# Kernel tuning notes

Hardware: AMD Instinct MI355X
Metric: run time of the kernel (lower is better)

## Reference

```python
import jax, jax.numpy as jnp
import numpy as np
import math

N = 100000      # n_entities
C = 128         # channel
E = 600000      # n_edges
NNZ = 1000000   # interact_mat nnz
NU = 50000      # n_users
NREL = 25       # n_relations
H = 4           # n_heads
DK = C // H     # d_k


def setup_inputs() -> dict:
    key = jax.random.key(0)
    ks = jax.random.split(key, 13)
    s = 1.0 / math.sqrt(C)
    return {
        "entity_emb": jax.random.normal(ks[0], (N, C), jnp.float32),
        "W_Q": jax.random.normal(ks[1], (C, C), jnp.float32) * s,
        "W_K": jax.random.normal(ks[2], (C, C), jnp.float32) * s,
        "W_V": jax.random.normal(ks[3], (C, C), jnp.float32) * s,
        "W_O": jax.random.normal(ks[4], (C, C), jnp.float32) * s,
        "relation_att": jax.random.normal(ks[5], (NREL - 1, H, DK, DK), jnp.float32) * s,
        "relation_msg": jax.random.normal(ks[6], (NREL - 1, H, DK, DK), jnp.float32) * s,
        "relation_emb": jax.random.normal(ks[7], (NREL - 1, C), jnp.float32),
        "edge_index": jax.random.randint(ks[8], (2, E), 0, N, jnp.int32),
        "edge_type": jax.random.randint(ks[9], (E,), 1, NREL, jnp.int32),
        "im_rows": jax.random.randint(ks[10], (NNZ,), 0, NU, jnp.int32),
        "im_cols": jax.random.randint(ks[11], (NNZ,), 0, N, jnp.int32),
        "im_vals": jax.random.uniform(ks[12], (NNZ,), jnp.float32),
        "n_users": NU,
    }


def reference(entity_emb, W_Q, W_K, W_V, W_O, relation_att, relation_msg,
              relation_emb, edge_index, edge_type, im_rows, im_cols, im_vals,
              n_users):
    n_entities, channel = entity_emb.shape
    n_heads, d_k = H, channel // H
    head, tail = edge_index[0], edge_index[1]
    rel = edge_type - 1

    # Step 1: heterogeneous mutual attention
    q = (entity_emb[head] @ W_Q).reshape(-1, n_heads, d_k)            # [E,H,Dk]
    k = (entity_emb[tail] @ W_K).reshape(-1, n_heads, d_k)
    k = jnp.einsum("ehd,ehdk->ehk", k, relation_att[rel])
    score = (q * k).sum(-1) / math.sqrt(d_k)                           # [E,H]

    # Step 2: heterogeneous message passing
    v = (entity_emb[tail] @ W_V).reshape(-1, n_heads, d_k)
    v = jnp.einsum("ehd,ehdk->ehk", v, relation_msg[rel])

    # scatter_softmax over target node id (head)
    seg_max = jax.ops.segment_max(score, head, num_segments=n_entities)  # [N,H]
    ex = jnp.exp(score - seg_max[head])
    denom = jax.ops.segment_sum(ex, head, num_segments=n_entities)
    attn = ex / denom[head]                                              # [E,H]

    agg = (v * attn[..., None]).reshape(-1, n_heads * d_k) @ W_O         # [E,C]
    entity_agg = jax.ops.segment_sum(agg, head, num_segments=n_entities)

    # user aggregate: sparse [NU,N] @ entity_emb
    user_agg = jax.ops.segment_sum(entity_emb[im_cols] * im_vals[:, None],
                                   im_rows, num_segments=n_users)
    return entity_agg, user_agg
```

## Files before the change

### kernel.cpp

```cpp
#include <hip/hip_runtime.h>
#include <hip/hip_bf16.h>
#include <math.h>

typedef __attribute__((ext_vector_type(8))) unsigned short u16x8;
typedef __attribute__((ext_vector_type(4))) unsigned short u16x4;
typedef __attribute__((ext_vector_type(8))) short bf16x8;
typedef __attribute__((ext_vector_type(4))) float f32x4;

#define NRELMAX 32

__device__ __forceinline__ float b2f(unsigned short u) {
    return __uint_as_float(((unsigned)u) << 16);
}
__device__ __forceinline__ unsigned short f2b(float v) {
    __hip_bfloat16 b = __float2bfloat16(v);
    return *reinterpret_cast<unsigned short*>(&b);
}

__device__ __forceinline__ bf16x8 lda_frag(const __hip_bfloat16* p) {
    return *(const bf16x8*)p;
}
__device__ __forceinline__ void st_o(__hip_bfloat16* p, float v) { *p = __float2bfloat16(v); }
__device__ __forceinline__ void st_o(float* p, float v) { *p = v; }

template <typename TO>
__global__ __launch_bounds__(256) void mfma_gemm(const __hip_bfloat16* __restrict__ A,
                                                 const __hip_bfloat16* __restrict__ Wt,
                                                 TO* __restrict__ out, int n)
{
    const int tid = threadIdx.x;
    const int w = tid >> 6;
    const int l = tid & 63;
    const int q = l >> 4;
    const int c16 = l & 15;
    const int wr = (w >> 1) * 64;
    const int wc = (w & 1) * 64;
    const long row0 = (long)blockIdx.x * 128;

    f32x4 acc[4][4] = {};
    #pragma unroll
    for (int ks = 0; ks < 4; ++ks) {
        bf16x8 af[4];
        #pragma unroll
        for (int rb = 0; rb < 4; ++rb) {
            long r = row0 + wr + rb * 16 + c16;
            if (r >= n) r = n - 1;
            af[rb] = lda_frag(A + r * 128 + ks * 32 + q * 8);
        }
        #pragma unroll
        for (int cb = 0; cb < 4; ++cb) {
            bf16x8 wf = *(const bf16x8*)(Wt + (size_t)(wc + cb * 16 + c16) * 128 + ks * 32 + q * 8);
            #pragma unroll
            for (int rb = 0; rb < 4; ++rb)
                acc[rb][cb] = __builtin_amdgcn_mfma_f32_16x16x32_bf16(af[rb], wf, acc[rb][cb], 0, 0, 0);
        }
    }
    #pragma unroll
    for (int rb = 0; rb < 4; ++rb) {
        #pragma unroll
        for (int r = 0; r < 4; ++r) {
            long row = row0 + wr + rb * 16 + q * 4 + r;
            if (row < n) {
                #pragma unroll
                for (int cb = 0; cb < 4; ++cb)
                    st_o(out + row * 128 + wc + cb * 16 + c16, acc[rb][cb][r]);
            }
        }
    }
}

__global__ __launch_bounds__(256) void trans_w4(
    const float* __restrict__ W0, const float* __restrict__ W1,
    const float* __restrict__ W2, const float* __restrict__ W3,
    __hip_bfloat16* __restrict__ T0, __hip_bfloat16* __restrict__ T1,
    __hip_bfloat16* __restrict__ T2, __hip_bfloat16* __restrict__ T3)
{
    int t = blockIdx.x * 256 + threadIdx.x;
    int w = t >> 14, r = t & 16383;
    const float* W = (w == 0) ? W0 : (w == 1) ? W1 : (w == 2) ? W2 : W3;
    __hip_bfloat16* T = (w == 0) ? T0 : (w == 1) ? T1 : (w == 2) ? T2 : T3;
    int k = r >> 7, c = r & 127;
    T[(size_t)c * 128 + k] = __float2bfloat16(W[(size_t)k * 128 + c]);
}

__global__ __launch_bounds__(256) void conv_emb(const float* __restrict__ emb,
                                                __hip_bfloat16* __restrict__ embb, long n4)
{
    long i = ((long)blockIdx.x * 256 + threadIdx.x) * 4;
    if (i >= n4 * 4) return;
    float4 v = *(const float4*)(emb + i);
    u16x4 o;
    o[0] = f2b(v.x); o[1] = f2b(v.y); o[2] = f2b(v.z); o[3] = f2b(v.w);
    *(u16x4*)(embb + i) = o;
}

__global__ __launch_bounds__(256) void conv_tab(const float* __restrict__ att,
                                                const float* __restrict__ msg,
                                                __hip_bfloat16* __restrict__ Atab,
                                                __hip_bfloat16* __restrict__ Mtab, int nrel)
{
    int t = blockIdx.x * 256 + threadIdx.x;
    int tot = nrel * 4096;
    if (t >= 2 * tot) return;
    const float* src = (t < tot) ? att : msg;
    __hip_bfloat16* dst = (t < tot) ? Atab : Mtab;
    int u = (t < tot) ? t : t - tot;
    int rel = u >> 12, rem = u & 4095;
    int h = rem >> 10;  rem &= 1023;
    int s2 = rem >> 9;  rem &= 511;
    int lane = rem >> 3, j = rem & 7;
    int g = lane >> 4, c = lane & 15;
    dst[u] = __float2bfloat16(src[(size_t)rel * 4096 + h * 1024 + s2 * 16 + (g * 8 + j) * 32 + c]);
}

__global__ __launch_bounds__(256) void count_rec(
    const int* __restrict__ head, const int* __restrict__ etyp,
    const int* __restrict__ irow,
    unsigned* __restrict__ ecnt8, unsigned* __restrict__ ucnt8,
    unsigned* __restrict__ rcnt, int* __restrict__ plocalE,
    int* __restrict__ plocalU, int E, int NNZ, int Np, int NUp)
{
    __shared__ unsigned lcnt[NRELMAX];
    const int tid = threadIdx.x;
    if (tid < NRELMAX) lcnt[tid] = 0;
    __syncthreads();
    int i = blockIdx.x * 256 + tid;
    unsigned rep = (unsigned)(blockIdx.x & 7);
    if (i < E) {
        unsigned p = atomicAdd(&ecnt8[rep * Np + head[i]], 1u);
        plocalE[i] = (int)(p | (rep << 28));
        atomicAdd(&lcnt[etyp[i] - 1], 1u);
    }
    if (i < NNZ) {
        unsigned p = atomicAdd(&ucnt8[rep * NUp + irow[i]], 1u);
        plocalU[i] = (int)(p | (rep << 28));
    }
    __syncthreads();
    if (tid < NRELMAX) {
        unsigned c = lcnt[tid];
        if (c) atomicAdd(&rcnt[tid], c);
    }
}

__global__ __launch_bounds__(256) void sum_rep(const unsigned* __restrict__ cnt8,
                                               unsigned* __restrict__ tot, int n, int stride)
{
    int i = blockIdx.x * 256 + threadIdx.x;
    if (i >= n) return;
    unsigned t = 0;
    #pragma unroll
    for (int r = 0; r < 8; ++r) t += cnt8[(size_t)r * stride + i];
    tot[i] = t;
}

__global__ __launch_bounds__(256) void mk_repbase(unsigned* __restrict__ cnt8,
                                                  const unsigned* __restrict__ base,
                                                  int n, int stride)
{
    int i = blockIdx.x * 256 + threadIdx.x;
    if (i >= n) return;
    unsigned acc = base[i];
    #pragma unroll
    for (int r = 0; r < 8; ++r) {
        unsigned c = cnt8[(size_t)r * stride + i];
        cnt8[(size_t)r * stride + i] = acc;
        acc += c;
    }
}

__global__ void rel_scan(const unsigned* __restrict__ rcnt, unsigned* __restrict__ rcur,
                         unsigned* __restrict__ rend, unsigned* __restrict__ rnext, int nrel)
{
    if (threadIdx.x == 0 && blockIdx.x == 0) {
        unsigned acc = 0;
        for (int r = 0; r < nrel; ++r) {
            rcur[r] = acc;
            rend[r] = acc + rcnt[r];
            acc += (rcnt[r] + 15u) & ~15u;
            rnext[r] = acc;
        }
    }
}

__global__ __launch_bounds__(256) void fill_pads(const unsigned* __restrict__ rend,
                                                 const unsigned* __restrict__ rnext,
                                                 int4* __restrict__ emeta, int nrel, long emax)
{
    for (int r = 0; r < nrel; ++r) {
        unsigned s = rend[r], e2 = rnext[r];
        for (unsigned i = s + threadIdx.x; i < e2; i += 256)
            emeta[i] = make_int4(0, 0, -1, r);
    }
    long ep = rnext[nrel - 1];
    for (long i = ep + threadIdx.x; i < emax; i += 256)
        emeta[i] = make_int4(0, 0, -1, nrel - 1);
}

__global__ __launch_bounds__(1024) void scan1(const unsigned* __restrict__ in,
                                              unsigned* __restrict__ out,
                                              unsigned* __restrict__ bsum, int n)
{
    __shared__ unsigned sh[1024];
    int i = blockIdx.x * 1024 + threadIdx.x;
    unsigned v = (i < n) ? in[i] : 0u;
    sh[threadIdx.x] = v;
    __syncthreads();
    for (int off = 1; off < 1024; off <<= 1) {
        unsigned t = (threadIdx.x >= (unsigned)off) ? sh[threadIdx.x - off] : 0u;
        __syncthreads();
        sh[threadIdx.x] += t;
        __syncthreads();
    }
    if (i < n) out[i] = sh[threadIdx.x] - v;
    if (threadIdx.x == 1023) bsum[blockIdx.x] = sh[1023];
}

__global__ __launch_bounds__(1024) void scan2(unsigned* __restrict__ bsum, int nb)
{
    __shared__ unsigned sh[1024];
    unsigned v = (threadIdx.x < (unsigned)nb) ? bsum[threadIdx.x] : 0u;
    sh[threadIdx.x] = v;
    __syncthreads();
    for (int off = 1; off < 1024; off <<= 1) {
        unsigned t = (threadIdx.x >= (unsigned)off) ? sh[threadIdx.x - off] : 0u;
        __syncthreads();
        sh[threadIdx.x] += t;
        __syncthreads();
    }
    if (threadIdx.x < (unsigned)nb) bsum[threadIdx.x] = sh[threadIdx.x] - v;
}

__global__ __launch_bounds__(1024) void scan3(unsigned* __restrict__ out,
                                              const unsigned* __restrict__ bsum, int n)
{
    int i = blockIdx.x * 1024 + threadIdx.x;
    if (i < n) out[i] += bsum[blockIdx.x];
}

__global__ __launch_bounds__(256) void fill_user2(const int* __restrict__ irow,
                                                  const int* __restrict__ icol,
                                                  const float* __restrict__ ival,
                                                  const unsigned* __restrict__ repbaseU,
                                                  const int* __restrict__ plocalU,
                                                  int2* __restrict__ upair, int n, int NUp)
{
    int i = blockIdx.x * 256 + threadIdx.x;
    if (i >= n) return;
    unsigned pl = (unsigned)plocalU[i];
    unsigned rep = pl >> 28;
    unsigned pos = pl & 0x0FFFFFFFu;
    unsigned slot = repbaseU[(size_t)rep * NUp + irow[i]] + pos;
    upair[slot] = make_int2(icol[i], __float_as_int(ival[i]));
}

__global__ __launch_bounds__(256) void fill_both2(const int* __restrict__ head,
                                                  const int* __restrict__ tail,
                                                  const int* __restrict__ etyp,
                                                  const unsigned* __restrict__ repbaseE,
                                                  const int* __restrict__ plocalE,
                                                  unsigned* __restrict__ rcur,
                                                  int4* __restrict__ emeta, int n, int Np)
{
    __shared__ unsigned lcnt[NRELMAX];
    __shared__ unsigned lbase[NRELMAX];
    const int tid = threadIdx.x;
    if (tid < NRELMAX) lcnt[tid] = 0;
    __syncthreads();
    int i = blockIdx.x * 256 + tid;
    int r = 0;
    unsigned lpos = 0;
    if (i < n) {
        r = etyp[i] - 1;
        lpos = atomicAdd(&lcnt[r], 1u);
    }
    __syncthreads();
    if (tid < NRELMAX) {
        unsigned c = lcnt[tid];
        lbase[tid] = c ? atomicAdd(&rcur[tid], c) : 0u;
    }
    __syncthreads();
    if (i < n) {
        unsigned pl = (unsigned)plocalE[i];
        unsigned rep = pl >> 28;
        unsigned pos = pl & 0x0FFFFFFFu;
        int hn = head[i];
        unsigned slot = repbaseE[(size_t)rep * Np + hn] + pos;
        emeta[lbase[r] + lpos] = make_int4(hn, tail[i], (int)slot, r);
    }
}

template <int ROUND>
__global__ __launch_bounds__(256, 2) void edge_pass(
    const __hip_bfloat16* __restrict__ Qb, const __hip_bfloat16* __restrict__ Kb,
    const __hip_bfloat16* __restrict__ Vb,
    const __hip_bfloat16* __restrict__ Atab, const __hip_bfloat16* __restrict__ Mtab,
    const int4* __restrict__ emeta, float* __restrict__ SC,
    __hip_bfloat16* __restrict__ VPh, long Epad, int chunk)
{
    const int wv = (blockIdx.x * 256 + threadIdx.x) >> 6;
    const int l = threadIdx.x & 63;
    const int g = l >> 4;
    const int c = l & 15;
    long j0 = (long)wv * chunk;
    if (j0 >= Epad) return;
    long j1 = j0 + chunk; if (j1 > Epad) j1 = Epad;

    bf16x8 aK[2][2], aM[2][2];
    int currel = -1;
    for (long pos = j0; pos < j1; pos += 16) {
        const int4 md = emeta[pos + c];
        const int rel0 = __shfl(md.w, 0, 64);
        if (rel0 != currel) {
            currel = rel0;
            #pragma unroll
            for (int hl = 0; hl < 2; ++hl) {
                const int h = ROUND * 2 + hl;
                #pragma unroll
                for (int s2 = 0; s2 < 2; ++s2) {
                    size_t idx = ((((size_t)rel0 * 4 + h) * 2 + s2) * 64 + l) * 8;
                    aK[hl][s2] = *(const bf16x8*)(Atab + idx);
                    aM[hl][s2] = *(const bf16x8*)(Mtab + idx);
                }
            }
        }
        const int tn = md.y, hn = md.x, slot = md.z;
        #pragma unroll
        for (int hl = 0; hl < 2; ++hl) {
            const int h = ROUND * 2 + hl;
            bf16x8 bk = *(const bf16x8*)(Kb + (size_t)tn * 128 + h * 32 + g * 8);
            bf16x8 bv = *(const bf16x8*)(Vb + (size_t)tn * 128 + h * 32 + g * 8);
            f32x4 z = {0.f, 0.f, 0.f, 0.f};
            f32x4 klo = __builtin_amdgcn_mfma_f32_16x16x32_bf16(aK[hl][0], bk, z, 0, 0, 0);
            f32x4 khi = __builtin_amdgcn_mfma_f32_16x16x32_bf16(aK[hl][1], bk, z, 0, 0, 0);
            f32x4 vlo = __builtin_amdgcn_mfma_f32_16x16x32_bf16(aM[hl][0], bv, z, 0, 0, 0);
            f32x4 vhi = __builtin_amdgcn_mfma_f32_16x16x32_bf16(aM[hl][1], bv, z, 0, 0, 0);
            const __hip_bfloat16* qp = Qb + (size_t)hn * 128 + h * 32;
            u16x4 q1 = *(const u16x4*)(qp + g * 4);
            u16x4 q2 = *(const u16x4*)(qp + 16 + g * 4);
            float p = 0.f;
            #pragma unroll
            for (int r = 0; r < 4; ++r)
                p += b2f(q1[r]) * klo[r] + b2f(q2[r]) * khi[r];
            p += __shfl_xor(p, 16, 64);
            p += __shfl_xor(p, 32, 64);
            if (slot >= 0) {
                if (g == 0) SC[(size_t)slot * 4 + h] = p * 0.17677669529663687f;
                u16x4 plo, phi;
                #pragma unroll
                for (int r = 0; r < 4; ++r) { plo[r] = f2b(vlo[r]); phi[r] = f2b(vhi[r]); }
                __hip_bfloat16* dst = VPh + (size_t)slot * 64 + hl * 32;
                *(u16x4*)(dst + g * 4) = plo;
                *(u16x4*)(dst + 16 + g * 4) = phi;
            }
        }
    }
}

template <int ROUND>
__global__ __launch_bounds__(256) void node_pass(
    const float* __restrict__ SC, const __hip_bfloat16* __restrict__ VPh,
    const unsigned* __restrict__ estart, __hip_bfloat16* __restrict__ M, int n, int Etot)
{
    int node = (blockIdx.x * 256 + threadIdx.x) >> 6;
    if (node >= n) return;
    int l = threadIdx.x & 63;
    int half = l >> 5;
    const int h = ROUND * 2 + half;
    unsigned beg = estart[node];
    unsigned end = (node + 1 < n) ? estart[node + 1] : (unsigned)Etot;
    float mx = -INFINITY, dn = 0.f;
    for (unsigned j = beg; j < end; ++j) {
        float s = SC[(size_t)j * 4 + h];
        float m2 = fmaxf(mx, s);
        dn = dn * __expf(mx - m2) + __expf(s - m2);
        mx = m2;
    }
    float inv = (end > beg) ? 1.f / dn : 0.f;
    float acc = 0.f;
    for (unsigned j = beg; j < end; ++j) {
        float w = __expf(SC[(size_t)j * 4 + h] - mx) * inv;
        acc = fmaf(w, __bfloat162float(VPh[(size_t)j * 64 + l]), acc);
    }
    M[(size_t)node * 128 + ROUND * 64 + l] = __float2bfloat16(acc);
}

__global__ __launch_bounds__(256) void user_gather(
    const __hip_bfloat16* __restrict__ embb, const unsigned* __restrict__ ustart,
    const int2* __restrict__ upair, float* __restrict__ out, int nu, int NNZ)
{
    int u = (blockIdx.x * 256 + threadIdx.x) >> 5;
    if (u >= nu) return;
    int l = threadIdx.x & 31;
    unsigned beg = ustart[u];
    unsigned end = (u + 1 < nu) ? ustart[u + 1] : (unsigned)NNZ;
    float a0 = 0.f, a1 = 0.f, a2 = 0.f, a3 = 0.f;
    float b0 = 0.f, b1 = 0.f, b2 = 0.f, b3 = 0.f;
    unsigned j = beg;
    for (; j + 3 < end; j += 4) {
        int2 p0 = upair[j], p1 = upair[j + 1], p2 = upair[j + 2], p3 = upair[j + 3];
        float v0 = __int_as_float(p0.y), v1 = __int_as_float(p1.y);
        float v2 = __int_as_float(p2.y), v3 = __int_as_float(p3.y);
        uint2 e0 = *(const uint2*)((const unsigned*)(embb + (size_t)p0.x * 128) + l * 2);
        uint2 e1 = *(const uint2*)((const unsigned*)(embb + (size_t)p1.x * 128) + l * 2);
        uint2 e2 = *(const uint2*)((const unsigned*)(embb + (size_t)p2.x * 128) + l * 2);
        uint2 e3 = *(const uint2*)((const unsigned*)(embb + (size_t)p3.x * 128) + l * 2);
        a0 = fmaf(b2f((unsigned short)(e0.x & 0xFFFF)), v0, a0);
        a1 = fmaf(b2f((unsigned short)(e0.x >> 16)), v0, a1);
        a2 = fmaf(b2f((unsigned short)(e0.y & 0xFFFF)), v0, a2);
        a3 = fmaf(b2f((unsigned short)(e0.y >> 16)), v0, a3);
        b0 = fmaf(b2f((unsigned short)(e1.x & 0xFFFF)), v1, b0);
        b1 = fmaf(b2f((unsigned short)(e1.x >> 16)), v1, b1);
        b2 = fmaf(b2f((unsigned short)(e1.y & 0xFFFF)), v1, b2);
        b3 = fmaf(b2f((unsigned short)(e1.y >> 16)), v1, b3);
        a0 = fmaf(b2f((unsigned short)(e2.x & 0xFFFF)), v2, a0);
        a1 = fmaf(b2f((unsigned short)(e2.x >> 16)), v2, a1);
        a2 = fmaf(b2f((unsigned short)(e2.y & 0xFFFF)), v2, a2);
        a3 = fmaf(b2f((unsigned short)(e2.y >> 16)), v2, a3);
        b0 = fmaf(b2f((unsigned short)(e3.x & 0xFFFF)), v3, b0);
        b1 = fmaf(b2f((unsigned short)(e3.x >> 16)), v3, b1);
        b2 = fmaf(b2f((unsigned short)(e3.y & 0xFFFF)), v3, b2);
        b3 = fmaf(b2f((unsigned short)(e3.y >> 16)), v3, b3);
    }
    for (; j < end; ++j) {
        int2 p0 = upair[j];
        float v0 = __int_as_float(p0.y);
        uint2 e0 = *(const uint2*)((const unsigned*)(embb + (size_t)p0.x * 128) + l * 2);
        a0 = fmaf(b2f((unsigned short)(e0.x & 0xFFFF)), v0, a0);
        a1 = fmaf(b2f((unsigned short)(e0.x >> 16)), v0, a1);
        a2 = fmaf(b2f((unsigned short)(e0.y & 0xFFFF)), v0, a2);
        a3 = fmaf(b2f((unsigned short)(e0.y >> 16)), v0, a3);
    }
    *(float4*)(out + (size_t)u * 128 + l * 4) =
        make_float4(a0 + b0, a1 + b1, a2 + b2, a3 + b3);
}

extern "C" void kernel_launch(void* const* d_in, const int* in_sizes, int n_in,
                              void* d_out, int out_size, void* d_ws, size_t ws_size,
                              hipStream_t stream)
{
    const float* emb = (const float*)d_in[0];
    const float* W_Q = (const float*)d_in[1];
    const float* W_K = (const float*)d_in[2];
    const float* W_V = (const float*)d_in[3];
    const float* W_O = (const float*)d_in[4];
    const float* att = (const float*)d_in[5];
    const float* msg = (const float*)d_in[6];
    const int* eidx  = (const int*)d_in[8];
    const int* etyp  = (const int*)d_in[9];
    const int* irow  = (const int*)d_in[10];
    const int* icol  = (const int*)d_in[11];
    const float* ival = (const float*)d_in[12];

    const int N    = in_sizes[0] / 128;
    const int E    = in_sizes[8] / 2;
    const int NNZ  = in_sizes[10];
    const int NU   = out_size / 128 - N;
    const int NREL = in_sizes[5] / 4096;

    const int* head = eidx;
    const int* tail = eidx + E;

    const int Np  = (N + 255) & ~255;
    const int NUp = (NU + 255) & ~255;

    const size_t NC = (size_t)N * 128;
    char* p = (char*)d_ws;
    __hip_bfloat16* VPh = (__hip_bfloat16*)p; p += (size_t)E * 64 * 2;
    __hip_bfloat16* Kb  = (__hip_bfloat16*)p; p += NC * 2;
    __hip_bfloat16* Vb  = (__hip_bfloat16*)p; p += NC * 2;
    __hip_bfloat16* M   = (__hip_bfloat16*)p; p += NC * 2;
    unsigned* rcnt  = (unsigned*)p; p += 32 * 4;
    unsigned* rcur  = (unsigned*)p; p += 32 * 4;
    unsigned* rend  = (unsigned*)p; p += 32 * 4;
    unsigned* rnext = (unsigned*)p; p += 32 * 4;
    unsigned* ucnt  = (unsigned*)p; p += (size_t)NUp * 4;
    unsigned* bsum  = (unsigned*)p; p += 1024 * 4;
    unsigned* bsumU = (unsigned*)p; p += 1024 * 4;
    int2* upair     = (int2*)p;     p += (size_t)NNZ * 8;
    __hip_bfloat16* WtQ = (__hip_bfloat16*)p; p += 16384 * 2;
    __hip_bfloat16* WtK = (__hip_bfloat16*)p; p += 16384 * 2;
    __hip_bfloat16* WtV = (__hip_bfloat16*)p; p += 16384 * 2;
    __hip_bfloat16* WtO = (__hip_bfloat16*)p; p += 16384 * 2;
    __hip_bfloat16* Atab = (__hip_bfloat16*)p; p += (size_t)NREL * 4096 * 2;
    __hip_bfloat16* Mtab = (__hip_bfloat16*)p; p += (size_t)NREL * 4096 * 2;

    int* plocalU     = (int*)VPh;
    int* plocalE     = plocalU + NNZ;
    unsigned* ucnt8  = (unsigned*)(plocalE + E);
    unsigned* ecnt8  = ucnt8 + (size_t)8 * NUp;

    float* out_ent = (float*)d_out;
    float* out_usr = out_ent + NC;
    __hip_bfloat16* embb = (__hip_bfloat16*)out_ent;
    __hip_bfloat16* Qb   = (__hip_bfloat16*)((char*)d_out + NC * 2);
    const long Emax = E + 512;
    float* SC   = out_usr;
    int4* emeta = (int4*)(out_usr + (size_t)E * 4);
    unsigned* ecnt = (unsigned*)((char*)emeta + (size_t)Emax * 16);

    hipMemsetAsync(rcnt, 0, 32 * 4, stream);
    hipMemsetAsync(ucnt8, 0, ((size_t)8 * NUp + (size_t)8 * Np) * 4, stream);

    trans_w4<<<256, 256, 0, stream>>>(W_Q, W_K, W_V, W_O, WtQ, WtK, WtV, WtO);
    conv_emb<<<(int)((NC / 4 + 255) / 256), 256, 0, stream>>>(emb, embb, (long)(NC / 4));
    conv_tab<<<(2 * NREL * 4096 + 255) / 256, 256, 0, stream>>>(att, msg, Atab, Mtab, NREL);

    int gg = (N + 127) / 128;
    mfma_gemm<__hip_bfloat16><<<gg, 256, 0, stream>>>(embb, WtQ, Qb, N);
    mfma_gemm<__hip_bfloat16><<<gg, 256, 0, stream>>>(embb, WtK, Kb, N);
    mfma_gemm<__hip_bfloat16><<<gg, 256, 0, stream>>>(embb, WtV, Vb, N);

    int gmax = ((NNZ > E ? NNZ : E) + 255) / 256;
    count_rec<<<gmax, 256, 0, stream>>>(head, etyp, irow, ecnt8, ucnt8, rcnt,
                                        plocalE, plocalU, E, NNZ, Np, NUp);
    rel_scan<<<1, 64, 0, stream>>>(rcnt, rcur, rend, rnext, NREL);
    fill_pads<<<1, 256, 0, stream>>>(rend, rnext, emeta, NREL, Emax);

    sum_rep<<<(N + 255) / 256, 256, 0, stream>>>(ecnt8, ecnt, N, Np);
    sum_rep<<<(NU + 255) / 256, 256, 0, stream>>>(ucnt8, ucnt, NU, NUp);
    int nbE = (N + 1023) / 1024;
    scan1<<<nbE, 1024, 0, stream>>>(ecnt, ecnt, bsum, N);
    scan2<<<1, 1024, 0, stream>>>(bsum, nbE);
    scan3<<<nbE, 1024, 0, stream>>>(ecnt, bsum, N);
    int nbU = (NU + 1023) / 1024;
    scan1<<<nbU, 1024, 0, stream>>>(ucnt, ucnt, bsumU, NU);
    scan2<<<1, 1024, 0, stream>>>(bsumU, nbU);
    scan3<<<nbU, 1024, 0, stream>>>(ucnt, bsumU, NU);
    mk_repbase<<<(N + 255) / 256, 256, 0, stream>>>(ecnt8, ecnt, N, Np);
    mk_repbase<<<(NU + 255) / 256, 256, 0, stream>>>(ucnt8, ucnt, NU, NUp);

    fill_user2<<<(NNZ + 255) / 256, 256, 0, stream>>>(irow, icol, ival, ucnt8,
                                                      plocalU, upair, NNZ, NUp);
    fill_both2<<<(E + 255) / 256, 256, 0, stream>>>(head, tail, etyp, ecnt8,
                                                    plocalE, rcur, emeta, E, Np);

    const int NWAVE = 16384;
    int chunk = (int)(((Emax + NWAVE - 1) / NWAVE + 15) & ~15L);
    edge_pass<0><<<NWAVE / 4, 256, 0, stream>>>(Qb, Kb, Vb, Atab, Mtab, emeta, SC, VPh, Emax, chunk);
    node_pass<0><<<(N + 3) / 4, 256, 0, stream>>>(SC, VPh, ecnt, M, N, E);
    edge_pass<1><<<NWAVE / 4, 256, 0, stream>>>(Qb, Kb, Vb, Atab, Mtab, emeta, SC, VPh, Emax, chunk);
    node_pass<1><<<(N + 3) / 4, 256, 0, stream>>>(SC, VPh, ecnt, M, N, E);

    user_gather<<<(NU + 7) / 8, 256, 0, stream>>>(embb, ucnt, upair, out_usr, NU, NNZ);

    mfma_gemm<float><<<gg, 256, 0, stream>>>(M, WtO, out_ent, N);
}
```

Before: 637.0 us.

## Fuse preprocessing, QKV GEMMs, scans and fills into fewer launches

Fuses the weight transpose, relation-table conversion, embedding bf16 conversion and edge/user counting into one block-partitioned kernel. The three QKV GEMMs become a single launch, and the multi-kernel block scans plus the relation scan become one three-block scan kernel. The user and edge fills and the pad fill are merged into one kernel. It also drops the 8-way replicated counters in favour of direct atomics on the count arrays. The goal is to cut launch count and the extra replica-sum passes, at the cost of more atomic contention and a serial single-block scan per array.

```diff
diff --git a/kernel.cpp b/kernel.cpp
--- a/kernel.cpp
+++ b/kernel.cpp
@@ -1,6 +1,7 @@
 #include <hip/hip_runtime.h>
 #include <hip/hip_bf16.h>
 #include <math.h>
+
 
 typedef __attribute__((ext_vector_type(8))) unsigned short u16x8;
 typedef __attribute__((ext_vector_type(4))) unsigned short u16x4;
@@ -24,9 +25,9 @@
 __device__ __forceinline__ void st_o(float* p, float v) { *p = v; }
 
 template <typename TO>
-__global__ __launch_bounds__(256) void mfma_gemm(const __hip_bfloat16* __restrict__ A,
-                                                 const __hip_bfloat16* __restrict__ Wt,
-                                                 TO* __restrict__ out, int n)
+__device__ __forceinline__ void gemm_body(const __hip_bfloat16* __restrict__ A,
+                                          const __hip_bfloat16* __restrict__ Wt,
+                                          TO* __restrict__ out, int n, int blk)
 {
     const int tid = threadIdx.x;
     const int w = tid >> 6;
@@ -35,7 +36,7 @@
     const int c16 = l & 15;
     const int wr = (w >> 1) * 64;
     const int wc = (w & 1) * 64;
-    const long row0 = (long)blockIdx.x * 128;
+    const long row0 = (long)blk * 128;
 
     f32x4 acc[4][4] = {};
     #pragma unroll
@@ -69,71 +70,91 @@
     }
 }
 
-__global__ __launch_bounds__(256) void trans_w4(
+template <typename TO>
+__global__ __launch_bounds__(256) void mfma_gemm(const __hip_bfloat16* __restrict__ A,
+                                                 const __hip_bfloat16* __restrict__ Wt,
+                                                 TO* __restrict__ out, int n)
+{
+    gemm_body<TO>(A, Wt, out, n, blockIdx.x);
+}
+
+__global__ __launch_bounds__(256) void qkv3(const __hip_bfloat16* __restrict__ A,
+                                            const __hip_bfloat16* __restrict__ WtQ,
+                                            const __hip_bfloat16* __restrict__ WtK,
+                                            const __hip_bfloat16* __restrict__ WtV,
+                                            __hip_bfloat16* __restrict__ Qb,
+                                            __hip_bfloat16* __restrict__ Kb,
+                                            __hip_bfloat16* __restrict__ Vb, int n, int gg)
+{
+    int which = blockIdx.x / gg;
+    int blk = blockIdx.x % gg;
+    const __hip_bfloat16* Wt = (which == 0) ? WtQ : (which == 1) ? WtK : WtV;
+    __hip_bfloat16* Out = (which == 0) ? Qb : (which == 1) ? Kb : Vb;
+    gemm_body<__hip_bfloat16>(A, Wt, Out, n, blk);
+}
+
+__global__ __launch_bounds__(256) void prep_count(
     const float* __restrict__ W0, const float* __restrict__ W1,
     const float* __restrict__ W2, const float* __restrict__ W3,
     __hip_bfloat16* __restrict__ T0, __hip_bfloat16* __restrict__ T1,
-    __hip_bfloat16* __restrict__ T2, __hip_bfloat16* __restrict__ T3)
-{
-    int t = blockIdx.x * 256 + threadIdx.x;
-    int w = t >> 14, r = t & 16383;
-    const float* W = (w == 0) ? W0 : (w == 1) ? W1 : (w == 2) ? W2 : W3;
-    __hip_bfloat16* T = (w == 0) ? T0 : (w == 1) ? T1 : (w == 2) ? T2 : T3;
-    int k = r >> 7, c = r & 127;
-    T[(size_t)c * 128 + k] = __float2bfloat16(W[(size_t)k * 128 + c]);
-}
-
-__global__ __launch_bounds__(256) void conv_emb(const float* __restrict__ emb,
-                                                __hip_bfloat16* __restrict__ embb, long n4)
-{
-    long i = ((long)blockIdx.x * 256 + threadIdx.x) * 4;
-    if (i >= n4 * 4) return;
-    float4 v = *(const float4*)(emb + i);
-    u16x4 o;
-    o[0] = f2b(v.x); o[1] = f2b(v.y); o[2] = f2b(v.z); o[3] = f2b(v.w);
-    *(u16x4*)(embb + i) = o;
-}
-
-__global__ __launch_bounds__(256) void conv_tab(const float* __restrict__ att,
-                                                const float* __restrict__ msg,
-                                                __hip_bfloat16* __restrict__ Atab,
-                                                __hip_bfloat16* __restrict__ Mtab, int nrel)
-{
-    int t = blockIdx.x * 256 + threadIdx.x;
-    int tot = nrel * 4096;
-    if (t >= 2 * tot) return;
-    const float* src = (t < tot) ? att : msg;
-    __hip_bfloat16* dst = (t < tot) ? Atab : Mtab;
-    int u = (t < tot) ? t : t - tot;
-    int rel = u >> 12, rem = u & 4095;
-    int h = rem >> 10;  rem &= 1023;
-    int s2 = rem >> 9;  rem &= 511;
-    int lane = rem >> 3, j = rem & 7;
-    int g = lane >> 4, c = lane & 15;
-    dst[u] = __float2bfloat16(src[(size_t)rel * 4096 + h * 1024 + s2 * 16 + (g * 8 + j) * 32 + c]);
-}
-
-__global__ __launch_bounds__(256) void count_rec(
+    __hip_bfloat16* __restrict__ T2, __hip_bfloat16* __restrict__ T3,
+    const float* __restrict__ att, const float* __restrict__ msg,
+    __hip_bfloat16* __restrict__ Atab, __hip_bfloat16* __restrict__ Mtab, int nrel,
+    const float* __restrict__ emb, __hip_bfloat16* __restrict__ embb, long n4,
     const int* __restrict__ head, const int* __restrict__ etyp,
     const int* __restrict__ irow,
-    unsigned* __restrict__ ecnt8, unsigned* __restrict__ ucnt8,
+    unsigned* __restrict__ ecnt, unsigned* __restrict__ ucnt,
     unsigned* __restrict__ rcnt, int* __restrict__ plocalE,
-    int* __restrict__ plocalU, int E, int NNZ, int Np, int NUp)
+    int* __restrict__ plocalU, int E, int NNZ,
+    int nbW, int nbT, int nbC)
 {
     __shared__ unsigned lcnt[NRELMAX];
     const int tid = threadIdx.x;
+    const int bx = blockIdx.x;
+    if (bx < nbW) {
+        int t = bx * 256 + tid;
+        int w = t >> 14, r = t & 16383;
+        const float* W = (w == 0) ? W0 : (w == 1) ? W1 : (w == 2) ? W2 : W3;
+        __hip_bfloat16* T = (w == 0) ? T0 : (w == 1) ? T1 : (w == 2) ? T2 : T3;
+        int k = r >> 7, c = r & 127;
+        T[(size_t)c * 128 + k] = __float2bfloat16(W[(size_t)k * 128 + c]);
+        return;
+    }
+    if (bx < nbW + nbT) {
+        int t = (bx - nbW) * 256 + tid;
+        int tot = nrel * 4096;
+        if (t >= 2 * tot) return;
+        const float* src = (t < tot) ? att : msg;
+        __hip_bfloat16* dst = (t < tot) ? Atab : Mtab;
+        int u = (t < tot) ? t : t - tot;
+        int rel = u >> 12, rem = u & 4095;
+        int h = rem >> 10;  rem &= 1023;
+        int s2 = rem >> 9;  rem &= 511;
+        int lane = rem >> 3, j = rem & 7;
+        int g = lane >> 4, c = lane & 15;
+        dst[u] = __float2bfloat16(src[(size_t)rel * 4096 + h * 1024 + s2 * 16 + (g * 8 + j) * 32 + c]);
+        return;
+    }
+    if (bx < nbW + nbT + nbC) {
+        long i = ((long)(bx - nbW - nbT) * 256 + tid) * 4;
+        if (i >= n4 * 4) return;
+        float4 v = *(const float4*)(emb + i);
+        u16x4 o;
+        o[0] = f2b(v.x); o[1] = f2b(v.y); o[2] = f2b(v.z); o[3] = f2b(v.w);
+        *(u16x4*)(embb + i) = o;
+        return;
+    }
     if (tid < NRELMAX) lcnt[tid] = 0;
     __syncthreads();
-    int i = blockIdx.x * 256 + tid;
-    unsigned rep = (unsigned)(blockIdx.x & 7);
+    int i = (bx - nbW - nbT - nbC) * 256 + tid;
     if (i < E) {
-        unsigned p = atomicAdd(&ecnt8[rep * Np + head[i]], 1u);
-        plocalE[i] = (int)(p | (rep << 28));
+        unsigned p = atomicAdd(&ecnt[head[i]], 1u);
+        plocalE[i] = (int)p;
         atomicAdd(&lcnt[etyp[i] - 1], 1u);
     }
     if (i < NNZ) {
-        unsigned p = atomicAdd(&ucnt8[rep * NUp + irow[i]], 1u);
-        plocalU[i] = (int)(p | (rep << 28));
+        unsigned p = atomicAdd(&ucnt[irow[i]], 1u);
+        plocalU[i] = (int)p;
     }
     __syncthreads();
     if (tid < NRELMAX) {
@@ -142,151 +163,102 @@
     }
 }
 
-__global__ __launch_bounds__(256) void sum_rep(const unsigned* __restrict__ cnt8,
-                                               unsigned* __restrict__ tot, int n, int stride)
-{
-    int i = blockIdx.x * 256 + threadIdx.x;
-    if (i >= n) return;
-    unsigned t = 0;
-    #pragma unroll
-    for (int r = 0; r < 8; ++r) t += cnt8[(size_t)r * stride + i];
-    tot[i] = t;
-}
-
-__global__ __launch_bounds__(256) void mk_repbase(unsigned* __restrict__ cnt8,
-                                                  const unsigned* __restrict__ base,
-                                                  int n, int stride)
-{
-    int i = blockIdx.x * 256 + threadIdx.x;
-    if (i >= n) return;
-    unsigned acc = base[i];
-    #pragma unroll
-    for (int r = 0; r < 8; ++r) {
-        unsigned c = cnt8[(size_t)r * stride + i];
-        cnt8[(size_t)r * stride + i] = acc;
-        acc += c;
-    }
-}
-
-__global__ void rel_scan(const unsigned* __restrict__ rcnt, unsigned* __restrict__ rcur,
-                         unsigned* __restrict__ rend, unsigned* __restrict__ rnext, int nrel)
-{
-    if (threadIdx.x == 0 && blockIdx.x == 0) {
-        unsigned acc = 0;
-        for (int r = 0; r < nrel; ++r) {
-            rcur[r] = acc;
-            rend[r] = acc + rcnt[r];
-            acc += (rcnt[r] + 15u) & ~15u;
-            rnext[r] = acc;
-        }
-    }
-}
-
-__global__ __launch_bounds__(256) void fill_pads(const unsigned* __restrict__ rend,
-                                                 const unsigned* __restrict__ rnext,
-                                                 int4* __restrict__ emeta, int nrel, long emax)
-{
-    for (int r = 0; r < nrel; ++r) {
-        unsigned s = rend[r], e2 = rnext[r];
-        for (unsigned i = s + threadIdx.x; i < e2; i += 256)
-            emeta[i] = make_int4(0, 0, -1, r);
-    }
-    long ep = rnext[nrel - 1];
-    for (long i = ep + threadIdx.x; i < emax; i += 256)
-        emeta[i] = make_int4(0, 0, -1, nrel - 1);
-}
-
-__global__ __launch_bounds__(1024) void scan1(const unsigned* __restrict__ in,
-                                              unsigned* __restrict__ out,
-                                              unsigned* __restrict__ bsum, int n)
-{
+__global__ __launch_bounds__(1024) void scan_all(
+    unsigned* __restrict__ ecnt, int n_e, unsigned* __restrict__ ucnt, int n_u,
+    const unsigned* __restrict__ rcnt, unsigned* __restrict__ rcur,
+    unsigned* __restrict__ rend, unsigned* __restrict__ rnext, int nrel)
+{
+    if (blockIdx.x == 2) {
+        if (threadIdx.x == 0) {
+            unsigned acc = 0;
+            for (int r = 0; r < nrel; ++r) {
+                rcur[r] = acc;
+                rend[r] = acc + rcnt[r];
+                acc += (rcnt[r] + 15u) & ~15u;
+                rnext[r] = acc;
+            }
+        }
+        return;
+    }
+    unsigned* buf = (blockIdx.x == 0) ? ecnt : ucnt;
+    int n = (blockIdx.x == 0) ? n_e : n_u;
     __shared__ unsigned sh[1024];
-    int i = blockIdx.x * 1024 + threadIdx.x;
-    unsigned v = (i < n) ? in[i] : 0u;
-    sh[threadIdx.x] = v;
+    const int tid = threadIdx.x;
+    int per = (n + 1023) >> 10;
+    int beg = tid * per;
+    int end = beg + per; if (end > n) end = n;
+    unsigned s = 0;
+    for (int i = beg; i < end && i < n; ++i) s += buf[i];
+    sh[tid] = s;
     __syncthreads();
     for (int off = 1; off < 1024; off <<= 1) {
-        unsigned t = (threadIdx.x >= (unsigned)off) ? sh[threadIdx.x - off] : 0u;
+        unsigned t = (tid >= off) ? sh[tid - off] : 0u;
         __syncthreads();
-        sh[threadIdx.x] += t;
+        sh[tid] += t;
         __syncthreads();
     }
-    if (i < n) out[i] = sh[threadIdx.x] - v;
-    if (threadIdx.x == 1023) bsum[blockIdx.x] = sh[1023];
-}
-
-__global__ __launch_bounds__(1024) void scan2(unsigned* __restrict__ bsum, int nb)
-{
-    __shared__ unsigned sh[1024];
-    unsigned v = (threadIdx.x < (unsigned)nb) ? bsum[threadIdx.x] : 0u;
-    sh[threadIdx.x] = v;
-    __syncthreads();
-    for (int off = 1; off < 1024; off <<= 1) {
-        unsigned t = (threadIdx.x >= (unsigned)off) ? sh[threadIdx.x - off] : 0u;
-        __syncthreads();
-        sh[threadIdx.x] += t;
-        __syncthreads();
-    }
-    if (threadIdx.x < (unsigned)nb) bsum[threadIdx.x] = sh[threadIdx.x] - v;
-}
-
-__global__ __launch_bounds__(1024) void scan3(unsigned* __restrict__ out,
-                                              const unsigned* __restrict__ bsum, int n)
-{
-    int i = blockIdx.x * 1024 + threadIdx.x;
-    if (i < n) out[i] += bsum[blockIdx.x];
-}
-
-__global__ __launch_bounds__(256) void fill_user2(const int* __restrict__ irow,
-                                                  const int* __restrict__ icol,
-                                                  const float* __restrict__ ival,
-                                                  const unsigned* __restrict__ repbaseU,
-                                                  const int* __restrict__ plocalU,
-                                                  int2* __restrict__ upair, int n, int NUp)
-{
-    int i = blockIdx.x * 256 + threadIdx.x;
-    if (i >= n) return;
-    unsigned pl = (unsigned)plocalU[i];
-    unsigned rep = pl >> 28;
-    unsigned pos = pl & 0x0FFFFFFFu;
-    unsigned slot = repbaseU[(size_t)rep * NUp + irow[i]] + pos;
-    upair[slot] = make_int2(icol[i], __float_as_int(ival[i]));
-}
-
-__global__ __launch_bounds__(256) void fill_both2(const int* __restrict__ head,
-                                                  const int* __restrict__ tail,
-                                                  const int* __restrict__ etyp,
-                                                  const unsigned* __restrict__ repbaseE,
-                                                  const int* __restrict__ plocalE,
-                                                  unsigned* __restrict__ rcur,
-                                                  int4* __restrict__ emeta, int n, int Np)
+    unsigned run = sh[tid] - s;
+    for (int i = beg; i < end && i < n; ++i) {
+        unsigned c = buf[i];
+        buf[i] = run;
+        run += c;
+    }
+}
+
+__global__ __launch_bounds__(256) void fills(
+    const int* __restrict__ irow, const int* __restrict__ icol,
+    const float* __restrict__ ival, const unsigned* __restrict__ ustart,
+    const int* __restrict__ plocalU, int2* __restrict__ upair, int NNZ,
+    const int* __restrict__ head, const int* __restrict__ tail,
+    const int* __restrict__ etyp, const unsigned* __restrict__ estart,
+    const int* __restrict__ plocalE, unsigned* __restrict__ rcur,
+    int4* __restrict__ emeta, int E,
+    const unsigned* __restrict__ rend, const unsigned* __restrict__ rnext,
+    int nrel, long emax, int nbU, int nbE)
 {
     __shared__ unsigned lcnt[NRELMAX];
     __shared__ unsigned lbase[NRELMAX];
     const int tid = threadIdx.x;
-    if (tid < NRELMAX) lcnt[tid] = 0;
-    __syncthreads();
-    int i = blockIdx.x * 256 + tid;
-    int r = 0;
-    unsigned lpos = 0;
-    if (i < n) {
-        r = etyp[i] - 1;
-        lpos = atomicAdd(&lcnt[r], 1u);
-    }
-    __syncthreads();
-    if (tid < NRELMAX) {
-        unsigned c = lcnt[tid];
-        lbase[tid] = c ? atomicAdd(&rcur[tid], c) : 0u;
-    }
-    __syncthreads();
-    if (i < n) {
-        unsigned pl = (unsigned)plocalE[i];
-        unsigned rep = pl >> 28;
-        unsigned pos = pl & 0x0FFFFFFFu;
-        int hn = head[i];
-        unsigned slot = repbaseE[(size_t)rep * Np + hn] + pos;
-        emeta[lbase[r] + lpos] = make_int4(hn, tail[i], (int)slot, r);
-    }
+    const int bx = blockIdx.x;
+    if (bx < nbU) {
+        int i = bx * 256 + tid;
+        if (i < NNZ) {
+            unsigned slot = ustart[irow[i]] + (unsigned)plocalU[i];
+            upair[slot] = make_int2(icol[i], __float_as_int(ival[i]));
+        }
+        return;
+    }
+    if (bx < nbU + nbE) {
+        if (tid < NRELMAX) lcnt[tid] = 0;
+        __syncthreads();
+        int i = (bx - nbU) * 256 + tid;
+        int r = 0;
+        unsigned lpos = 0;
+        if (i < E) {
+            r = etyp[i] - 1;
+            lpos = atomicAdd(&lcnt[r], 1u);
+        }
+        __syncthreads();
+        if (tid < NRELMAX) {
+            unsigned c = lcnt[tid];
+            lbase[tid] = c ? atomicAdd(&rcur[tid], c) : 0u;
+        }
+        __syncthreads();
+        if (i < E) {
+            int hn = head[i];
+            unsigned slot = estart[hn] + (unsigned)plocalE[i];
+            emeta[lbase[r] + lpos] = make_int4(hn, tail[i], (int)slot, r);
+        }
+        return;
+    }
+    for (int r = 0; r < nrel; ++r) {
+        unsigned s = rend[r], e2 = rnext[r];
+        for (unsigned i = s + tid; i < e2; i += 256)
+            emeta[i] = make_int4(0, 0, -1, r);
+    }
+    long ep = rnext[nrel - 1];
+    for (long i = ep + tid; i < emax; i += 256)
+        emeta[i] = make_int4(0, 0, -1, nrel - 1);
 }
 
 template <int ROUND>
@@ -460,7 +432,6 @@
     const int* head = eidx;
     const int* tail = eidx + E;
 
-    const int Np  = (N + 255) & ~255;
     const int NUp = (NU + 255) & ~255;
 
     const size_t NC = (size_t)N * 128;
@@ -474,8 +445,6 @@
     unsigned* rend  = (unsigned*)p; p += 32 * 4;
     unsigned* rnext = (unsigned*)p; p += 32 * 4;
     unsigned* ucnt  = (unsigned*)p; p += (size_t)NUp * 4;
-    unsigned* bsum  = (unsigned*)p; p += 1024 * 4;
-    unsigned* bsumU = (unsigned*)p; p += 1024 * 4;
     int2* upair     = (int2*)p;     p += (size_t)NNZ * 8;
     __hip_bfloat16* WtQ = (__hip_bfloat16*)p; p += 16384 * 2;
     __hip_bfloat16* WtK = (__hip_bfloat16*)p; p += 16384 * 2;
@@ -484,10 +453,8 @@
     __hip_bfloat16* Atab = (__hip_bfloat16*)p; p += (size_t)NREL * 4096 * 2;
     __hip_bfloat16* Mtab = (__hip_bfloat16*)p; p += (size_t)NREL * 4096 * 2;
 
-    int* plocalU     = (int*)VPh;
-    int* plocalE     = plocalU + NNZ;
-    unsigned* ucnt8  = (unsigned*)(plocalE + E);
-    unsigned* ecnt8  = ucnt8 + (size_t)8 * NUp;
+    int* plocalU = (int*)VPh;
+    int* plocalE = plocalU + NNZ;
 
     float* out_ent = (float*)d_out;
     float* out_usr = out_ent + NC;
@@ -498,41 +465,31 @@
     int4* emeta = (int4*)(out_usr + (size_t)E * 4);
     unsigned* ecnt = (unsigned*)((char*)emeta + (size_t)Emax * 16);
 
-    hipMemsetAsync(rcnt, 0, 32 * 4, stream);
-    hipMemsetAsync(ucnt8, 0, ((size_t)8 * NUp + (size_t)8 * Np) * 4, stream);
-
-    trans_w4<<<256, 256, 0, stream>>>(W_Q, W_K, W_V, W_O, WtQ, WtK, WtV, WtO);
-    conv_emb<<<(int)((NC / 4 + 255) / 256), 256, 0, stream>>>(emb, embb, (long)(NC / 4));
-    conv_tab<<<(2 * NREL * 4096 + 255) / 256, 256, 0, stream>>>(att, msg, Atab, Mtab, NREL);
+    hipMemsetAsync(rcnt, 0, (32 * 4) * 4 + (size_t)NUp * 4, stream);
+    hipMemsetAsync(ecnt, 0, (size_t)N * 4, stream);
+
+    const int nbW = 256;
+    const int nbT = (2 * NREL * 4096 + 255) / 256;
+    const int nbC = (int)((NC / 4 + 255) / 256);
+    const int nbX = ((NNZ > E ? NNZ : E) + 255) / 256;
+    prep_count<<<nbW + nbT + nbC + nbX, 256, 0, stream>>>(
+        W_Q, W_K, W_V, W_O, WtQ, WtK, WtV, WtO,
+        att, msg, Atab, Mtab, NREL,
+        emb, embb, (long)(NC / 4),
+        head, etyp, irow, ecnt, ucnt, rcnt, plocalE, plocalU,
+        E, NNZ, nbW, nbT, nbC);
 
     int gg = (N + 127) / 128;
-    mfma_gemm<__hip_bfloat16><<<gg, 256, 0, stream>>>(embb, WtQ, Qb, N);
-    mfma_gemm<__hip_bfloat16><<<gg, 256, 0, stream>>>(embb, WtK, Kb, N);
-    mfma_gemm<__hip_bfloat16><<<gg, 256, 0, stream>>>(embb, WtV, Vb, N);
-
-    int gmax = ((NNZ > E ? NNZ : E) + 255) / 256;
-    count_rec<<<gmax, 256, 0, stream>>>(head, etyp, irow, ecnt8, ucnt8, rcnt,
-                                        plocalE, plocalU, E, NNZ, Np, NUp);
-    rel_scan<<<1, 64, 0, stream>>>(rcnt, rcur, rend, rnext, NREL);
-    fill_pads<<<1, 256, 0, stream>>>(rend, rnext, emeta, NREL, Emax);
-
-    sum_rep<<<(N + 255) / 256, 256, 0, stream>>>(ecnt8, ecnt, N, Np);
-    sum_rep<<<(NU + 255) / 256, 256, 0, stream>>>(ucnt8, ucnt, NU, NUp);
-    int nbE = (N + 1023) / 1024;
-    scan1<<<nbE, 1024, 0, stream>>>(ecnt, ecnt, bsum, N);
-    scan2<<<1, 1024, 0, stream>>>(bsum, nbE);
-    scan3<<<nbE, 1024, 0, stream>>>(ecnt, bsum, N);
-    int nbU = (NU + 1023) / 1024;
-    scan1<<<nbU, 1024, 0, stream>>>(ucnt, ucnt, bsumU, NU);
-    scan2<<<1, 1024, 0, stream>>>(bsumU, nbU);
-    scan3<<<nbU, 1024, 0, stream>>>(ucnt, bsumU, NU);
-    mk_repbase<<<(N + 255) / 256, 256, 0, stream>>>(ecnt8, ecnt, N, Np);
-    mk_repbase<<<(NU + 255) / 256, 256, 0, stream>>>(ucnt8, ucnt, NU, NUp);
-
-    fill_user2<<<(NNZ + 255) / 256, 256, 0, stream>>>(irow, icol, ival, ucnt8,
-                                                      plocalU, upair, NNZ, NUp);
-    fill_both2<<<(E + 255) / 256, 256, 0, stream>>>(head, tail, etyp, ecnt8,
-                                                    plocalE, rcur, emeta, E, Np);
+    qkv3<<<3 * gg, 256, 0, stream>>>(embb, WtQ, WtK, WtV, Qb, Kb, Vb, N, gg);
+
+    scan_all<<<3, 1024, 0, stream>>>(ecnt, N, ucnt, NU, rcnt, rcur, rend, rnext, NREL);
+
+    const int nbU = (NNZ + 255) / 256;
+    const int nbE = (E + 255) / 256;
+    fills<<<nbU + nbE + 1, 256, 0, stream>>>(
+        irow, icol, ival, ucnt, plocalU, upair, NNZ,
+        head, tail, etyp, ecnt, plocalE, rcur, emeta, E,
+        rend, rnext, NREL, Emax, nbU, nbE);
 
     const int NWAVE = 16384;
     int chunk = (int)(((Emax + NWAVE - 1) / NWAVE + 15) & ~15L);
```

Measured after the change: 735.0 us. 15.4% more time.
